# Optimization experiments

Hardware: AMD Instinct MI355X
Metric: run time of the kernel (lower is better)

The kernel has to match this reference:

```python
import jax, jax.numpy as jnp
import numpy as np

NG, NF, NW = 5, 10, 4
STEP = 1 + NG + NF            # 16 signatures per writer
B = NW * STEP                 # 64
T, DFEAT = 512, 64
GAMMA = 5.0                   # SoftDTW gamma
BANDWIDTH = 0.1               # Sakoe-Chiba band (|i-j| <= 0.1 -> diagonal only)
INF = 1e7                     # finite 'infinity' to keep grads NaN-free
ALPHA, BETA, P_W, R_W = 0.5, 1.0, 0.1, 0.1
MARGIN_MAX, MARGIN_MIN = 1.0, 0.1
K_NUM, K_MUL = 5, 2.0
SIZ = NW * (NW + 1) // 2      # 10 (buffer size in original code)


def setup_inputs() -> dict:
    key = jax.random.key(0)
    k1, k2 = jax.random.split(key)
    data = jax.random.normal(k1, (B, T, DFEAT), dtype=jnp.float32)
    teacher_data = jax.random.normal(k2, (B, T, DFEAT), dtype=jnp.float32)
    # equal lengths: the bandwidth=0.1 band only admits the main diagonal,
    # so only equal-length pairs yield finite SoftDTW values.
    lens = jnp.full((B,), T, dtype=jnp.int32)
    return {"data": data, "lens": lens, "teacher_data": teacher_data}


def sq_dist(X, Y):
    # X: [P,N,d], Y: [P,M,d] -> [P,N,M] squared euclidean cost (SoftDTW default)
    x2 = jnp.sum(X * X, -1)[:, :, None]
    y2 = jnp.sum(Y * Y, -1)[:, None, :]
    return x2 + y2 - 2.0 * jnp.einsum('bid,bjd->bij', X, Y)


def softdtw_batch(Dmat):
    # Batched SoftDTW via anti-diagonal wavefront scan. Dmat: [P,N,N].
    Pn, N, _ = Dmat.shape
    i = jnp.arange(N)
    k = jnp.arange(2 * N - 1)[:, None]            # diagonal index
    j = k - i[None, :]                            # [2N-1, N]
    valid = (j >= 0) & (j < N)
    inband = valid & (jnp.abs(i[None, :] - j) <= BANDWIDTH)
    jc = jnp.clip(j, 0, N - 1)
    Dg = Dmat[:, i[None, :], jc]                  # [P, 2N-1, N] diag-gathered costs
    Dg = jnp.moveaxis(Dg, 1, 0)                   # [2N-1, P, N]

    def step(carry, xs):
        Rp, Rp2 = carry                           # diagonals k-1, k-2; [P,N]
        Dk, mk, kk = xs
        pad = jnp.full((Pn, 1), INF, Dk.dtype)
        above = jnp.concatenate([pad, Rp[:, :-1]], axis=1)   # R[i-1, j]
        left = Rp                                             # R[i, j-1]
        diag = jnp.concatenate([pad, Rp2[:, :-1]], axis=1)   # R[i-1, j-1]
        stacked = jnp.stack([above, left, diag], axis=0)
        smin = -GAMMA * jax.nn.logsumexp(-stacked / GAMMA, axis=0)
        Rk = Dk + smin
        Rk = jnp.where(kk == 0, Dk, Rk)           # R[0,0] = D[0,0]
        Rk = jnp.where(mk[None, :], Rk, INF)      # outside band -> INF
        return (Rk, Rp), None

    init = (jnp.full((Pn, N), INF, Dmat.dtype), jnp.full((Pn, N), INF, Dmat.dtype))
    (Rlast, _), _ = jax.lax.scan(step, init, (Dg, inband, jnp.arange(2 * N - 1)))
    return Rlast[:, N - 1]                        # R[N-1, N-1]


def mmd_loss(src, tgt):
    # Literal multi-kernel Gaussian MMD applied to 3D [n,T,d] inputs:
    # torch broadcasting of ((total[None]-total[:,None])**2).sum(2) -> [2n,2n,d]
    n = src.shape[0]
    total = jnp.concatenate([src, tgt], axis=0)   # [2n, T, d]
    sq = jnp.sum(total * total, axis=1)           # [2n, d]
    cross = jnp.einsum('atd,btd->abd', total, total)
    L2 = sq[:, None, :] + sq[None, :, :] - 2.0 * cross
    ns = 2 * n
    bw = jax.lax.stop_gradient(jnp.sum(L2)) / (ns * ns - ns)  # .data in torch
    bw = bw / (K_MUL ** (K_NUM // 2))
    kernels = sum(jnp.exp(-L2 / (bw * (K_MUL ** ii))) for ii in range(K_NUM))
    XX, YY = kernels[:n, :n], kernels[n:, n:]
    XY, YX = kernels[:n, n:], kernels[n:, :n]
    return jnp.mean(XX + YY - XY - YX)


def reference(data, lens, teacher_data):
    lens_f = lens.astype(data.dtype)
    widx = jnp.arange(NW) * STEP
    a_idx = jnp.repeat(widx, NG + NF)                                   # anchors
    o_idx = (widx[:, None] + 1 + jnp.arange(NG + NF)[None, :]).reshape(-1)
    # batch student + teacher pairs into one SoftDTW call: [2P, T, T]
    X = jnp.concatenate([data[a_idx], teacher_data[a_idx]], axis=0)
    Y = jnp.concatenate([data[o_idx], teacher_data[o_idx]], axis=0)
    sd = softdtw_batch(sq_dist(X, Y))
    denom = lens_f[a_idx] + lens_f[o_idx]
    Pn = NW * (NG + NF)
    d_s = (sd[:Pn] / denom).reshape(NW, NG + NF)
    d_t = (sd[Pn:] / denom).reshape(NW, NG + NF)
    dist_g, dist_n = d_s[:, :NG], d_s[:, NG:]
    dist_g_t, dist_n_t = d_t[:, :NG], d_t[:, NG:]

    # teacher-driven dynamic margin
    dists_t = jax.nn.relu(dist_n_t[:, :, None] - dist_g_t[:, None, :])  # [NW,NF,NG]
    mx = jnp.max(dists_t, axis=(1, 2), keepdims=True)
    fd = (MARGIN_MAX - MARGIN_MIN) / mx * dists_t + MARGIN_MIN
    lk = jax.nn.relu(dist_g[:, None, :] - dist_n[:, :, None] + fd)
    nz = jax.lax.stop_gradient(jnp.sum(lk != 0, axis=(1, 2))).astype(lk.dtype)
    lv = jnp.sum(lk, axis=(1, 2)) / (nz + 1.0)
    ca = jnp.mean(dist_g, axis=1)
    cb = jnp.mean(dist_n[:, :5], axis=1)
    intra = jnp.sum(dist_g - ca[:, None], axis=1)
    inter = jax.nn.relu(BETA - jnp.abs(ca - cb))
    total_loss = jnp.mean(lv + intra * P_W + inter * R_W)

    # MMD over writer pairs, excluding last 5 (random forgeries)
    groups = data.reshape(NW, STEP, T, DFEAT)[:, :STEP - 5]             # [NW,11,T,d]
    pairs = [(i, j) for i in range(NW) for j in range(1, NW) if i != j]
    src = jnp.stack([groups[i] for i, _ in pairs])
    tgt = jnp.stack([groups[j] for _, j in pairs])
    mmd_vals = jax.vmap(mmd_loss)(src, tgt)
    mmds = jnp.zeros((SIZ,), data.dtype).at[:len(pairs)].set(mmd_vals)
    mmd1 = jnp.max(mmds) * ALPHA
    return total_loss + mmd1
```

## Files before the change

### kernel.cpp

```cpp
#include <hip/hip_runtime.h>
#include <math.h>

#define T_LEN 512
#define DF 64
#define ROW_ELEMS (T_LEN * DF)
#define STEP_ 16
#define NROWS_G 44
#define GSTRIDE (NROWS_G * DF)

__constant__ int c_PI[9] = {0, 0, 0, 1, 1, 2, 2, 3, 3};
__constant__ int c_PJ[9] = {1, 2, 3, 2, 3, 1, 3, 1, 2};

__device__ inline float blockSum(float v, float* tmp4) {
    #pragma unroll
    for (int off = 32; off > 0; off >>= 1) v += __shfl_down(v, off);
    if ((threadIdx.x & 63) == 0) tmp4[threadIdx.x >> 6] = v;
    __syncthreads();
    const float s = tmp4[0] + tmp4[1] + tmp4[2] + tmp4[3];
    __syncthreads();
    return s;
}

__global__ __launch_bounds__(1024) void k_pair(const float* __restrict__ data,
                                               const float* __restrict__ teacher,
                                               float* __restrict__ sd,
                                               float* __restrict__ G,
                                               unsigned* __restrict__ counter)
{
    const int b = blockIdx.x;
    const int tid = threadIdx.x;

    __shared__ float red2[16][16][DF];
    __shared__ float red[1024];

    if (b == 0 && tid == 0) *counter = 0u;

    if (b < 66) {
        int q = b, ta = 0;
        while (q >= 11 - ta) { q -= 11 - ta; ta++; }
        const int tb = ta + q;
        const int d = tid & 63, ty = tid >> 6;
        const int ua0 = ta * 4, ub0 = tb * 4;

        const float* rA[4];
        const float* rB[4];
        #pragma unroll
        for (int i = 0; i < 4; ++i) {
            const int ua = ua0 + i, ub = ub0 + i;
            rA[i] = data + (size_t)((ua / 11) * STEP_ + (ua % 11)) * ROW_ELEMS;
            rB[i] = data + (size_t)((ub / 11) * STEP_ + (ub % 11)) * ROW_ELEMS;
        }

        float acc[4][4];
        #pragma unroll
        for (int i = 0; i < 4; ++i)
            #pragma unroll
            for (int j = 0; j < 4; ++j) acc[i][j] = 0.f;

        #pragma unroll 2
        for (int t = ty; t < T_LEN; t += 16) {
            float av[4], bv[4];
            #pragma unroll
            for (int i = 0; i < 4; ++i) av[i] = rA[i][t * DF + d];
            #pragma unroll
            for (int j = 0; j < 4; ++j) bv[j] = rB[j][t * DF + d];
            #pragma unroll
            for (int i = 0; i < 4; ++i)
                #pragma unroll
                for (int j = 0; j < 4; ++j) acc[i][j] += av[i] * bv[j];
        }

        #pragma unroll
        for (int i = 0; i < 4; ++i)
            #pragma unroll
            for (int j = 0; j < 4; ++j) red2[ty][i * 4 + j][d] = acc[i][j];
        __syncthreads();

        const int ij = tid >> 6;
        const int i = ij >> 2, j = ij & 3;
        float s = 0.f;
        #pragma unroll
        for (int t2 = 0; t2 < 16; ++t2) s += red2[t2][ij][d];

        const int ua = ua0 + i, ub = ub0 + j;
        G[(size_t)ua * GSTRIDE + ub * DF + d] = s;
        G[(size_t)ub * GSTRIDE + ua * DF + d] = s;
    } else {
        const int bb = b - 66;
        const float* src = (bb < 60) ? data : teacher;
        const int p = bb % 60;
        const int w = p / 15, k = p % 15;
        const float4* A = (const float4*)(src + (size_t)(w * STEP_) * ROW_ELEMS);
        const float4* O = (const float4*)(src + (size_t)(w * STEP_ + 1 + k) * ROW_ELEMS);
        float acc = 0.f;
        #pragma unroll 4
        for (int i = tid; i < ROW_ELEMS / 4; i += 1024) {
            float4 a = A[i], o = O[i];
            float dx = a.x - o.x, dy = a.y - o.y, dz = a.z - o.z, dw = a.w - o.w;
            acc += dx * dx + dy * dy + dz * dz + dw * dw;
        }
        red[tid] = acc;
        __syncthreads();
        for (int s = 512; s > 0; s >>= 1) {
            if (tid < s) red[tid] += red[tid + s];
            __syncthreads();
        }
        if (tid == 0) sd[bb] = red[0];
    }
}

__global__ __launch_bounds__(256) void k_mmd2(const float* __restrict__ G,
                                              const float* __restrict__ sd,
                                              const int* __restrict__ lens,
                                              float* __restrict__ partial,
                                              unsigned* __restrict__ counter,
                                              float* __restrict__ out)
{
    const int blk = blockIdx.x;
    const int p = blk / 22, aa = blk % 22;
    const int tid = threadIdx.x;
    const int gi = c_PI[p], gj = c_PJ[p];

    __shared__ float diagT[22 * DF];
    __shared__ float tmp4[4];
    __shared__ float fin[256];
    __shared__ float mmd9[9];
    __shared__ float sdl[120];
    __shared__ int lastFlag;

    for (int e = tid; e < 22 * DF; e += 256) {
        const int bb = e >> 6, d2 = e & 63;
        const int ub = (bb < 11) ? gi * 11 + bb : gj * 11 + bb - 11;
        diagT[e] = G[(size_t)ub * GSTRIDE + ub * DF + d2];
    }

    float gs = 0.f;
    for (int e = tid; e < 7744; e += 256) {
        const int f4 = e % 176;
        const int sp = (e / 176) & 1;
        const int a2 = e / 352;
        const int ua = (a2 < 11) ? gi * 11 + a2 : gj * 11 + a2 - 11;
        const int colbase = (sp ? gj : gi) * 11 * DF;
        const float4 v = *(const float4*)(G + (size_t)ua * GSTRIDE + colbase + f4 * 4);
        gs += v.x + v.y + v.z + v.w;
    }
    __syncthreads();

    float dsp = 0.f;
    for (int e = tid; e < 22 * DF; e += 256) dsp += diagT[e];

    const float sumG    = blockSum(gs,  tmp4);
    const float diagSum = blockSum(dsp, tmp4);

    const float bw = (44.f * diagSum - 2.f * sumG) / (462.f * 4.f);
    const float inv0 = 1.f / bw;

    const int ua = (aa < 11) ? gi * 11 + aa : gj * 11 + aa - 11;
    const bool sa = (aa < 11);
    const float* crossRow = G + (size_t)ua * GSTRIDE;

    float s2 = 0.f;
    for (int e = tid; e < 22 * DF; e += 256) {
        const int bb = e >> 6, d2 = e & 63;
        const int ub = (bb < 11) ? gi * 11 + bb : gj * 11 + bb - 11;
        const float cr = crossRow[ub * DF + d2];
        const float l2 = diagT[aa * DF + d2] + diagT[e] - 2.f * cr;
        float kv = 0.f, inv = inv0;
        #pragma unroll
        for (int ii = 0; ii < 5; ++ii) { kv += __expf(-l2 * inv); inv *= 0.5f; }
        s2 += ((bb < 11) == sa) ? kv : -kv;
    }
    const float rowSum = blockSum(s2, tmp4);

    if (tid == 0) {
        partial[blk] = rowSum;
        __threadfence();
        const unsigned old = atomicAdd(counter, 1u);
        lastFlag = (old == 197u);
    }
    __syncthreads();
    if (!lastFlag) return;

    float pv = 0.f;
    if (tid < 198) pv = atomicAdd(&partial[tid], 0.f);
    fin[tid] = pv;
    __syncthreads();

    if (tid < 9) {
        float s = 0.f;
        #pragma unroll
        for (int k2 = 0; k2 < 22; ++k2) s += fin[tid * 22 + k2];
        mmd9[tid] = s / (121.f * 64.f);
    }
    if (tid < 120) sdl[tid] = sd[tid];
    __syncthreads();

    if (tid == 0) {
        float total = 0.f;
        for (int w = 0; w < 4; ++w) {
            float ds[15], dt[15];
            for (int k = 0; k < 15; ++k) {
                const float denom = (float)lens[w * STEP_] + (float)lens[w * STEP_ + 1 + k];
                ds[k] = sdl[w * 15 + k] / denom;
                dt[k] = sdl[60 + w * 15 + k] / denom;
            }
            float mx = 0.f;
            for (int i = 0; i < 10; ++i)
                for (int j = 0; j < 5; ++j) {
                    float v = dt[5 + i] - dt[j];
                    v = v > 0.f ? v : 0.f;
                    mx = fmaxf(mx, v);
                }
            const float scale = (1.0f - 0.1f) / mx;
            float sum_lk = 0.f, nz = 0.f;
            for (int i = 0; i < 10; ++i)
                for (int j = 0; j < 5; ++j) {
                    float v = dt[5 + i] - dt[j];
                    v = v > 0.f ? v : 0.f;
                    const float fd = scale * v + 0.1f;
                    float lk = ds[j] - ds[5 + i] + fd;
                    lk = lk > 0.f ? lk : 0.f;
                    sum_lk += lk;
                    if (lk != 0.f) nz += 1.f;
                }
            const float lv = sum_lk / (nz + 1.f);
            const float ca = (ds[0] + ds[1] + ds[2] + ds[3] + ds[4]) * 0.2f;
            const float cb = (ds[5] + ds[6] + ds[7] + ds[8] + ds[9]) * 0.2f;
            const float intra = (ds[0] - ca) + (ds[1] - ca) + (ds[2] - ca) + (ds[3] - ca) + (ds[4] - ca);
            float inter = 1.0f - fabsf(ca - cb);
            inter = inter > 0.f ? inter : 0.f;
            total += lv + intra * 0.1f + inter * 0.1f;
        }
        total *= 0.25f;

        float mmax = 0.f;
        for (int q = 0; q < 9; ++q) mmax = fmaxf(mmax, mmd9[q]);
        out[0] = total + 0.5f * mmax;
    }
}

extern "C" void kernel_launch(void* const* d_in, const int* in_sizes, int n_in,
                              void* d_out, int out_size, void* d_ws, size_t ws_size,
                              hipStream_t stream) {
    const float* data    = (const float*)d_in[0];
    const int*   lens    = (const int*)d_in[1];
    const float* teacher = (const float*)d_in[2];
    float* out = (float*)d_out;

    float*    sd      = (float*)d_ws;
    float*    G       = sd + 128;
    float*    partial = G + (size_t)NROWS_G * GSTRIDE;
    unsigned* counter = (unsigned*)(partial + 256);

    k_pair<<<186, 1024, 0, stream>>>(data, teacher, sd, G, counter);
    k_mmd2<<<9 * 22, 256, 0, stream>>>(G, sd, lens, partial, counter, out);
}
```

Baseline: 107.2 us.

## Split Gram tiles over time halves into two buffers with float4 loads

The pairwise Gram kernel now launches two blocks per tile, each covering half of the time axis and writing partial results to separate buffers G0/G1. Blocks shrink from 1024 to 256 threads, and each thread loads float4 vectors across four feature lanes. The MMD kernel adds the two partial buffers together when it reads them and processes the kernel sum in float4 chunks. This raises block count and memory parallelism on a grid that was underfilled, at the cost of a second Gram buffer and twice the reads in the second kernel.

```diff
diff --git a/kernel.cpp b/kernel.cpp
--- a/kernel.cpp
+++ b/kernel.cpp
@@ -21,72 +21,86 @@
     return s;
 }
 
-__global__ __launch_bounds__(1024) void k_pair(const float* __restrict__ data,
-                                               const float* __restrict__ teacher,
-                                               float* __restrict__ sd,
-                                               float* __restrict__ G,
-                                               unsigned* __restrict__ counter)
+__global__ __launch_bounds__(256) void k_pair(const float* __restrict__ data,
+                                              const float* __restrict__ teacher,
+                                              float* __restrict__ sd,
+                                              float* __restrict__ G0,
+                                              float* __restrict__ G1,
+                                              unsigned* __restrict__ counter)
 {
     const int b = blockIdx.x;
     const int tid = threadIdx.x;
 
     __shared__ float red2[16][16][DF];
-    __shared__ float red[1024];
+    __shared__ float redS[256];
 
     if (b == 0 && tid == 0) *counter = 0u;
 
-    if (b < 66) {
-        int q = b, ta = 0;
+    if (b < 132) {
+        const int tile = b >> 1, half = b & 1;
+        int q = tile, ta = 0;
         while (q >= 11 - ta) { q -= 11 - ta; ta++; }
         const int tb = ta + q;
-        const int d = tid & 63, ty = tid >> 6;
+        const int ty = tid >> 4, dq = tid & 15;
         const int ua0 = ta * 4, ub0 = tb * 4;
 
-        const float* rA[4];
-        const float* rB[4];
+        const float4* rA[4];
+        const float4* rB[4];
         #pragma unroll
         for (int i = 0; i < 4; ++i) {
             const int ua = ua0 + i, ub = ub0 + i;
-            rA[i] = data + (size_t)((ua / 11) * STEP_ + (ua % 11)) * ROW_ELEMS;
-            rB[i] = data + (size_t)((ub / 11) * STEP_ + (ub % 11)) * ROW_ELEMS;
-        }
-
-        float acc[4][4];
+            rA[i] = (const float4*)(data + (size_t)((ua / 11) * STEP_ + (ua % 11)) * ROW_ELEMS);
+            rB[i] = (const float4*)(data + (size_t)((ub / 11) * STEP_ + (ub % 11)) * ROW_ELEMS);
+        }
+
+        float acc[4][4][4];
         #pragma unroll
         for (int i = 0; i < 4; ++i)
             #pragma unroll
-            for (int j = 0; j < 4; ++j) acc[i][j] = 0.f;
-
+            for (int j = 0; j < 4; ++j)
+                #pragma unroll
+                for (int c = 0; c < 4; ++c) acc[i][j][c] = 0.f;
+
+        const int tbase = half * 256 + ty;
         #pragma unroll 2
-        for (int t = ty; t < T_LEN; t += 16) {
-            float av[4], bv[4];
-            #pragma unroll
-            for (int i = 0; i < 4; ++i) av[i] = rA[i][t * DF + d];
-            #pragma unroll
-            for (int j = 0; j < 4; ++j) bv[j] = rB[j][t * DF + d];
+        for (int it = 0; it < 16; ++it) {
+            const int t = tbase + it * 16;
+            float4 av[4], bv[4];
+            #pragma unroll
+            for (int i = 0; i < 4; ++i) av[i] = rA[i][t * 16 + dq];
+            #pragma unroll
+            for (int j = 0; j < 4; ++j) bv[j] = rB[j][t * 16 + dq];
             #pragma unroll
             for (int i = 0; i < 4; ++i)
                 #pragma unroll
-                for (int j = 0; j < 4; ++j) acc[i][j] += av[i] * bv[j];
+                for (int j = 0; j < 4; ++j) {
+                    acc[i][j][0] += av[i].x * bv[j].x;
+                    acc[i][j][1] += av[i].y * bv[j].y;
+                    acc[i][j][2] += av[i].z * bv[j].z;
+                    acc[i][j][3] += av[i].w * bv[j].w;
+                }
         }
 
         #pragma unroll
         for (int i = 0; i < 4; ++i)
             #pragma unroll
-            for (int j = 0; j < 4; ++j) red2[ty][i * 4 + j][d] = acc[i][j];
+            for (int j = 0; j < 4; ++j)
+                *(float4*)&red2[ty][i * 4 + j][dq * 4] =
+                    make_float4(acc[i][j][0], acc[i][j][1], acc[i][j][2], acc[i][j][3]);
         __syncthreads();
 
-        const int ij = tid >> 6;
-        const int i = ij >> 2, j = ij & 3;
-        float s = 0.f;
-        #pragma unroll
-        for (int t2 = 0; t2 < 16; ++t2) s += red2[t2][ij][d];
-
-        const int ua = ua0 + i, ub = ub0 + j;
-        G[(size_t)ua * GSTRIDE + ub * DF + d] = s;
-        G[(size_t)ub * GSTRIDE + ua * DF + d] = s;
+        float* __restrict__ Gh = half ? G1 : G0;
+        for (int o = tid; o < 1024; o += 256) {
+            const int ij = o >> 6, d = o & 63;
+            float s = 0.f;
+            #pragma unroll
+            for (int t2 = 0; t2 < 16; ++t2) s += red2[t2][ij][d];
+            const int ua = ua0 + (ij >> 2), ub = ub0 + (ij & 3);
+            Gh[(size_t)ua * GSTRIDE + ub * DF + d] = s;
+            Gh[(size_t)ub * GSTRIDE + ua * DF + d] = s;
+        }
     } else {
-        const int bb = b - 66;
+        const int bb = b - 132;
         const float* src = (bb < 60) ? data : teacher;
         const int p = bb % 60;
         const int w = p / 15, k = p % 15;
@@ -94,22 +108,23 @@
         const float4* O = (const float4*)(src + (size_t)(w * STEP_ + 1 + k) * ROW_ELEMS);
         float acc = 0.f;
         #pragma unroll 4
-        for (int i = tid; i < ROW_ELEMS / 4; i += 1024) {
+        for (int i = tid; i < ROW_ELEMS / 4; i += 256) {
             float4 a = A[i], o = O[i];
             float dx = a.x - o.x, dy = a.y - o.y, dz = a.z - o.z, dw = a.w - o.w;
             acc += dx * dx + dy * dy + dz * dz + dw * dw;
         }
-        red[tid] = acc;
+        redS[tid] = acc;
         __syncthreads();
-        for (int s = 512; s > 0; s >>= 1) {
-            if (tid < s) red[tid] += red[tid + s];
+        for (int s = 128; s > 0; s >>= 1) {
+            if (tid < s) redS[tid] += redS[tid + s];
             __syncthreads();
         }
-        if (tid == 0) sd[bb] = red[0];
-    }
-}
-
-__global__ __launch_bounds__(256) void k_mmd2(const float* __restrict__ G,
+        if (tid == 0) sd[bb] = redS[0];
+    }
+}
+
+__global__ __launch_bounds__(256) void k_mmd2(const float* __restrict__ G0,
+                                              const float* __restrict__ G1,
                                               const float* __restrict__ sd,
                                               const int* __restrict__ lens,
                                               float* __restrict__ partial,
@@ -131,9 +146,12 @@
     for (int e = tid; e < 22 * DF; e += 256) {
         const int bb = e >> 6, d2 = e & 63;
         const int ub = (bb < 11) ? gi * 11 + bb : gj * 11 + bb - 11;
-        diagT[e] = G[(size_t)ub * GSTRIDE + ub * DF + d2];
-    }
-
+        const size_t off = (size_t)ub * GSTRIDE + ub * DF + d2;
+        diagT[e] = G0[off] + G1[off];
+    }
+
+    const float4* G0q = (const float4*)G0;
+    const float4* G1q = (const float4*)G1;
     float gs = 0.f;
     for (int e = tid; e < 7744; e += 256) {
         const int f4 = e % 176;
@@ -141,8 +159,9 @@
         const int a2 = e / 352;
         const int ua = (a2 < 11) ? gi * 11 + a2 : gj * 11 + a2 - 11;
         const int colbase = (sp ? gj : gi) * 11 * DF;
-        const float4 v = *(const float4*)(G + (size_t)ua * GSTRIDE + colbase + f4 * 4);
-        gs += v.x + v.y + v.z + v.w;
+        const size_t qi = ((size_t)ua * GSTRIDE + colbase) / 4 + f4;
+        const float4 v0 = G0q[qi], v1 = G1q[qi];
+        gs += (v0.x + v1.x) + (v0.y + v1.y) + (v0.z + v1.z) + (v0.w + v1.w);
     }
     __syncthreads();
 
@@ -157,17 +176,29 @@
 
     const int ua = (aa < 11) ? gi * 11 + aa : gj * 11 + aa - 11;
     const bool sa = (aa < 11);
-    const float* crossRow = G + (size_t)ua * GSTRIDE;
+    const float4* cr0 = (const float4*)(G0 + (size_t)ua * GSTRIDE);
+    const float4* cr1 = (const float4*)(G1 + (size_t)ua * GSTRIDE);
+    const float4* dTq = (const float4*)diagT;
 
     float s2 = 0.f;
-    for (int e = tid; e < 22 * DF; e += 256) {
-        const int bb = e >> 6, d2 = e & 63;
+    for (int e = tid; e < 22 * 16; e += 256) {
+        const int bb = e >> 4, dq = e & 15;
         const int ub = (bb < 11) ? gi * 11 + bb : gj * 11 + bb - 11;
-        const float cr = crossRow[ub * DF + d2];
-        const float l2 = diagT[aa * DF + d2] + diagT[e] - 2.f * cr;
-        float kv = 0.f, inv = inv0;
-        #pragma unroll
-        for (int ii = 0; ii < 5; ++ii) { kv += __expf(-l2 * inv); inv *= 0.5f; }
+        const float4 c0 = cr0[ub * 16 + dq], c1 = cr1[ub * 16 + dq];
+        const float4 dB = dTq[e];
+        const float4 dA = dTq[aa * 16 + dq];
+        float l2[4];
+        l2[0] = dA.x + dB.x - 2.f * (c0.x + c1.x);
+        l2[1] = dA.y + dB.y - 2.f * (c0.y + c1.y);
+        l2[2] = dA.z + dB.z - 2.f * (c0.z + c1.z);
+        l2[3] = dA.w + dB.w - 2.f * (c0.w + c1.w);
+        float kv = 0.f;
+        #pragma unroll
+        for (int c = 0; c < 4; ++c) {
+            float inv = inv0;
+            #pragma unroll
+            for (int ii = 0; ii < 5; ++ii) { kv += __expf(-l2[c] * inv); inv *= 0.5f; }
+        }
         s2 += ((bb < 11) == sa) ? kv : -kv;
     }
     const float rowSum = blockSum(s2, tmp4);
@@ -234,7 +265,7 @@
         total *= 0.25f;
 
         float mmax = 0.f;
-        for (int q = 0; q < 9; ++q) mmax = fmaxf(mmax, mmd9[q]);
+        for (int q2 = 0; q2 < 9; ++q2) mmax = fmaxf(mmax, mmd9[q2]);
         out[0] = total + 0.5f * mmax;
     }
 }
@@ -248,10 +279,11 @@
     float* out = (float*)d_out;
 
     float*    sd      = (float*)d_ws;
-    float*    G       = sd + 128;
-    float*    partial = G + (size_t)NROWS_G * GSTRIDE;
+    float*    G0      = sd + 128;
+    float*    G1      = G0 + (size_t)NROWS_G * GSTRIDE;
+    float*    partial = G1 + (size_t)NROWS_G * GSTRIDE;
     unsigned* counter = (unsigned*)(partial + 256);
 
-    k_pair<<<186, 1024, 0, stream>>>(data, teacher, sd, G, counter);
-    k_mmd2<<<9 * 22, 256, 0, stream>>>(G, sd, lens, partial, counter, out);
-}
+    k_pair<<<252, 256, 0, stream>>>(data, teacher, sd, G0, G1, counter);
+    k_mmd2<<<9 * 22, 256, 0, stream>>>(G0, G1, sd, lens, partial, counter, out);
+}
```

Result: faster. 102.1 us (-4.8%).
